# Kernel tuning notes

Hardware: AMD Instinct MI355X
Metric: run time of the kernel (lower is better)

Reference implementation:

```python
import jax, jax.numpy as jnp
import numpy as np

EMBED_DIM = 1024
NUM_HEADS = 16
HEAD_DIM = EMBED_DIM // NUM_HEADS
B, S = 4, 2048


def setup_inputs() -> dict:
    key = jax.random.key(0)
    ks = jax.random.split(key, 11)
    sc = 1.0 / np.sqrt(EMBED_DIM)
    return {
        "query": jax.random.normal(ks[0], (B, S, EMBED_DIM), jnp.float32),
        "key": jax.random.normal(ks[1], (B, S, EMBED_DIM), jnp.float32),
        "value": jax.random.normal(ks[2], (B, S, EMBED_DIM), jnp.float32),
        "Wq": jax.random.normal(ks[3], (EMBED_DIM, EMBED_DIM), jnp.float32) * sc,
        "Wk": jax.random.normal(ks[4], (EMBED_DIM, EMBED_DIM), jnp.float32) * sc,
        "Wv": jax.random.normal(ks[5], (EMBED_DIM, EMBED_DIM), jnp.float32) * sc,
        "Wo": jax.random.normal(ks[6], (EMBED_DIM, EMBED_DIM), jnp.float32) * sc,
        "bq": jax.random.normal(ks[7], (EMBED_DIM,), jnp.float32) * 0.01,
        "bk": jax.random.normal(ks[8], (EMBED_DIM,), jnp.float32) * 0.01,
        "bv": jax.random.normal(ks[9], (EMBED_DIM,), jnp.float32) * 0.01,
        "bo": jax.random.normal(ks[10], (EMBED_DIM,), jnp.float32) * 0.01,
    }


def reference(query, key, value, Wq, Wk, Wv, Wo, bq, bk, bv, bo):
    # QKV projections: [B,S,E] @ [E,E] (torch Linear uses x @ W.T; here W stored pre-transposed)
    def split_heads(x):  # [B,S,E] -> [B,H,S,D]
        Bx, Sx, _ = x.shape
        return x.reshape(Bx, Sx, NUM_HEADS, HEAD_DIM).transpose(0, 2, 1, 3)

    Q = split_heads(query @ Wq + bq)
    K = split_heads(key @ Wk + bk)
    V = split_heads(value @ Wv + bv)

    scale = 1.0 / np.sqrt(HEAD_DIM).astype(np.float32)
    scores = jnp.einsum("bhqd,bhkd->bhqk", Q, K) * scale  # [B,H,Sq,Sk]
    attn = jax.nn.softmax(scores, axis=-1)
    ctx = jnp.einsum("bhqk,bhkd->bhqd", attn, V)  # [B,H,Sq,D]
    ctx = ctx.transpose(0, 2, 1, 3).reshape(query.shape[0], query.shape[1], EMBED_DIM)
    return ctx @ Wo + bo
```

## Files before the change

### kernel.cpp

```cpp
#include <hip/hip_runtime.h>
#include <hip/hip_bf16.h>

typedef unsigned short u16;
typedef unsigned int u32;
typedef __attribute__((ext_vector_type(8))) short bf16x8;
typedef __attribute__((ext_vector_type(4))) float f32x4;
typedef __attribute__((ext_vector_type(2))) unsigned u32x2v;

constexpr int Bn = 4;
constexpr int Sn = 2048;
constexpr int En = 1024;
constexpr int Hn = 16;
constexpr int Dn = 64;
constexpr int Kd = 1024;

__device__ __forceinline__ u16 f2b(float f) {
  union { float f; unsigned u; } v; v.f = f;
  unsigned u = v.u;
  return (u16)((u + 0x7fffu + ((u >> 16) & 1u)) >> 16);
}

__device__ __forceinline__ u32 cvtpk_bf16(float lo, float hi) {
  u32 r;
  asm("v_cvt_pk_bf16_f32 %0, %1, %2" : "=v"(r) : "v"(lo), "v"(hi));
  return r;
}

__device__ __forceinline__ void gl_lds16(const u16* g, u16* l) {
  __builtin_amdgcn_global_load_lds(
      (const __attribute__((address_space(1))) void*)g,
      (__attribute__((address_space(3))) void*)l, 16, 0, 0);
}

__device__ __forceinline__ void plchain(u32& a, u32& b) {
  u32x2v s = __builtin_amdgcn_permlane32_swap(a, b, false, false);
  u32x2v t = __builtin_amdgcn_permlane16_swap(s[0], s[1], false, false);
  a = t[0]; b = t[1];
}

__device__ __forceinline__ float redmax_cross(float r) {
  union { float f; u32 u; } v; v.f = r;
  u32x2v s = __builtin_amdgcn_permlane32_swap(v.u, v.u, false, false);
  union { u32 u; float f; } x, y;
  x.u = s[0]; y.u = s[1];
  float m = fmaxf(x.f, y.f);
  union { float f; u32 u; } w; w.f = m;
  u32x2v t = __builtin_amdgcn_permlane16_swap(w.u, w.u, false, false);
  x.u = t[0]; y.u = t[1];
  return fmaxf(x.f, y.f);
}
__device__ __forceinline__ float redsum_cross(float r) {
  union { float f; u32 u; } v; v.f = r;
  u32x2v s = __builtin_amdgcn_permlane32_swap(v.u, v.u, false, false);
  union { u32 u; float f; } x, y;
  x.u = s[0]; y.u = s[1];
  float m = x.f + y.f;
  union { float f; u32 u; } w; w.f = m;
  u32x2v t = __builtin_amdgcn_permlane16_swap(w.u, w.u, false, false);
  x.u = t[0]; y.u = t[1];
  return x.f + y.f;
}

__global__ __launch_bounds__(256) void conv_act(const float* __restrict__ in,
                                                u16* __restrict__ out, int n8) {
  int i = blockIdx.x * blockDim.x + threadIdx.x;
  const int stride = gridDim.x * blockDim.x;
  for (; i < n8; i += stride) {
    const float4* p = (const float4*)(in + (size_t)i * 8);
    float4 a = p[0], b = p[1];
    union { u32 w[4]; bf16x8 v; } r;
    r.w[0] = cvtpk_bf16(a.x, a.y); r.w[1] = cvtpk_bf16(a.z, a.w);
    r.w[2] = cvtpk_bf16(b.x, b.y); r.w[3] = cvtpk_bf16(b.z, b.w);
    *(bf16x8*)(out + (size_t)i * 8) = r.v;
  }
}

__global__ __launch_bounds__(256) void conv_wt(const float* __restrict__ W,
                                               u16* __restrict__ Wt) {
  __shared__ float ts[64][65];
  const int t = threadIdx.x;
  const int k0 = blockIdx.y * 64, n0 = blockIdx.x * 64;
  const int r = t >> 4, c4 = (t & 15) * 4;
  #pragma unroll
  for (int i = 0; i < 4; i++) {
    float4 v = *(const float4*)&W[(size_t)(k0 + i * 16 + r) * En + n0 + c4];
    ts[i * 16 + r][c4 + 0] = v.x;
    ts[i * 16 + r][c4 + 1] = v.y;
    ts[i * 16 + r][c4 + 2] = v.z;
    ts[i * 16 + r][c4 + 3] = v.w;
  }
  __syncthreads();
  const int n = t >> 2, kc = (t & 3) * 16;
  u32 w8[8];
  #pragma unroll
  for (int j = 0; j < 8; j++)
    w8[j] = cvtpk_bf16(ts[kc + 2 * j][n], ts[kc + 2 * j + 1][n]);
  *(bf16x8*)&Wt[(size_t)(n0 + n) * Kd + k0 + kc]     = *(bf16x8*)&w8[0];
  *(bf16x8*)&Wt[(size_t)(n0 + n) * Kd + k0 + kc + 8] = *(bf16x8*)&w8[4];
}

template<int OUT_MODE>
__global__ __launch_bounds__(256) void gemm_k(
    const u16* __restrict__ A, const u16* __restrict__ Bt,
    const float* __restrict__ biasp, void* __restrict__ Cp, float alpha)
{
  constexpr int BK = 64;
  __shared__ u16 As[128 * BK];
  __shared__ u16 Bs[128 * BK];
  const int tid = threadIdx.x;
  const int lane = tid & 63, wave = tid >> 6;
  const int brow = blockIdx.y * 128, bcol = blockIdx.x * 128;
  const int wrow = (wave >> 1) * 64, wcol = (wave & 1) * 64;
  const int fr = lane & 15, fk = (lane >> 4) * 8, rq = (lane >> 4) * 4;

  const int lr = lane >> 3, lc = (lane & 7) * 8;
  const u16* Ag = A  + (size_t)(brow + 32 * wave + lr) * Kd + lc;
  const u16* Bg = Bt + (size_t)(bcol + 32 * wave + lr) * Kd + lc;
  u16* Asw = &As[(32 * wave) * BK];
  u16* Bsw = &Bs[(32 * wave) * BK];

  f32x4 acc[4][4] = {};

  for (int kt = 0; kt < Kd; kt += BK) {
    __syncthreads();
    #pragma unroll
    for (int i = 0; i < 4; i++) {
      gl_lds16(Ag + kt + (size_t)(8 * i) * Kd, Asw + (8 * i) * BK);
      gl_lds16(Bg + kt + (size_t)(8 * i) * Kd, Bsw + (8 * i) * BK);
    }
    __syncthreads();
    bf16x8 af[4][2], bfv[4][2];
    #pragma unroll
    for (int m = 0; m < 4; m++)
      #pragma unroll
      for (int ks = 0; ks < 2; ks++)
        af[m][ks] = *(const bf16x8*)&As[(wrow + m * 16 + fr) * BK + ks * 32 + fk];
    #pragma unroll
    for (int n = 0; n < 4; n++)
      #pragma unroll
      for (int ks = 0; ks < 2; ks++)
        bfv[n][ks] = *(const bf16x8*)&Bs[(wcol + n * 16 + fr) * BK + ks * 32 + fk];
    #pragma unroll
    for (int ks = 0; ks < 2; ks++)
      #pragma unroll
      for (int m = 0; m < 4; m++)
        #pragma unroll
        for (int n = 0; n < 4; n++)
          acc[m][n] = __builtin_amdgcn_mfma_f32_16x16x32_bf16(af[m][ks], bfv[n][ks], acc[m][n], 0, 0, 0);
  }

  #pragma unroll
  for (int m = 0; m < 4; m++) {
    #pragma unroll
    for (int n = 0; n < 4; n++) {
      const int row0 = brow + wrow + m * 16 + rq;
      const int col  = bcol + wcol + n * 16 + fr;
      const float bi = biasp[col];
      if constexpr (OUT_MODE == 0) {
        #pragma unroll
        for (int j = 0; j < 4; j++)
          ((float*)Cp)[(size_t)(row0 + j) * En + col] = (acc[m][n][j] + bi) * alpha;
      } else if constexpr (OUT_MODE == 1) {
        #pragma unroll
        for (int j = 0; j < 4; j++)
          ((u16*)Cp)[(size_t)(row0 + j) * En + col] = f2b((acc[m][n][j] + bi) * alpha);
      } else {
        u16 t4[4];
        #pragma unroll
        for (int j = 0; j < 4; j++) t4[j] = f2b((acc[m][n][j] + bi) * alpha);
        int bb = row0 >> 11, s = row0 & (Sn - 1);
        int hh = col >> 6, d = col & (Dn - 1);
        uint2 pk;
        pk.x = (u32)t4[0] | ((u32)t4[1] << 16);
        pk.y = (u32)t4[2] | ((u32)t4[3] << 16);
        *(uint2*)&((u16*)Cp)[((size_t)(bb * Hn + hh) * Dn + d) * Sn + s] = pk;
      }
    }
  }
}

#define SWZ(row, unit) (((row) * 64) + ((((unit) ^ ((row) & 7))) * 8))

__global__ __launch_bounds__(256) void attn_k(
    const u16* __restrict__ Qw, const u16* __restrict__ Kw,
    const u16* __restrict__ Vt, u16* __restrict__ Cw)
{
  constexpr int KB = 64, NT = Sn / KB, TSZ = 64 * 64;
  __shared__ u16 Ks[2 * TSZ];
  __shared__ u16 Vs[3 * TSZ];
  const int tid = threadIdx.x, lane = tid & 63, wave = tid >> 6;
  const int id = blockIdx.x;
  const int bh = (id & 7) * 8 + (id >> 7);
  const int qb = (id >> 3) & 15;
  const int b = bh >> 4, h = bh & 15;
  const int qbase = qb * 128 + wave * 32;
  const int fr = lane & 15, fk = (lane >> 4) * 8, rq = (lane >> 4) * 4;
  const int g = lane >> 4;

  const u16* Qg  = Qw + (size_t)(b * Sn + qbase) * En + h * Dn;
  const u16* Kg0 = Kw + (size_t)(b * Sn) * En + h * Dn;
  const u16* Vg0 = Vt + (size_t)bh * Dn * Sn;

  bf16x8 qf[2][2];
  #pragma unroll
  for (int qm = 0; qm < 2; qm++)
    #pragma unroll
    for (int ds = 0; ds < 2; ds++)
      qf[qm][ds] = *(const bf16x8*)&Qg[(size_t)(qm * 16 + fr) * En + ds * 32 + fk];

  float mi_s[2] = {-INFINITY, -INFINITY};
  float li_s[2] = {0.f, 0.f};
  f32x4 o[2][4] = {};

  const int sr0 = 16 * wave + (lane >> 3);
  const int su  = (lane & 7);

  auto stageK = [&](int kv, int kb) {
    #pragma unroll
    for (int c = 0; c < 2; c++) {
      const int r = sr0 + 8 * c;
      const int u = su ^ (r & 7);
      gl_lds16(Kg0 + (size_t)(kv + r) * En + u * 8, &Ks[kb * TSZ + (16 * wave + 8 * c) * 64]);
    }
  };
  auto stageV = [&](int kv, int vb) {
    #pragma unroll
    for (int c = 0; c < 2; c++) {
      const int r = sr0 + 8 * c;
      const int u = su ^ (r & 7);
      gl_lds16(Vg0 + (size_t)r * Sn + kv + u * 8, &Vs[vb * TSZ + (16 * wave + 8 * c) * 64]);
    }
  };

  stageK(0, 0); stageV(0, 0);
  asm volatile("s_waitcnt vmcnt(0)" ::: "memory");
  __syncthreads();
  stageK(KB, 1); stageV(KB, 1);

  f32x4 stc[4][2] = {};
  #pragma unroll
  for (int kb = 0; kb < 4; kb++)
    #pragma unroll
    for (int ds = 0; ds < 2; ds++) {
      bf16x8 kf = *(const bf16x8*)&Ks[SWZ(kb * 16 + fr, ds * 4 + g)];
      #pragma unroll
      for (int qm = 0; qm < 2; qm++)
        stc[kb][qm] = __builtin_amdgcn_mfma_f32_16x16x32_bf16(kf, qf[qm][ds], stc[kb][qm], 0, 0, 0);
    }

  int vcur = 0, vfut = 2;

  for (int t = 0; t < NT; t++) {
    asm volatile("s_waitcnt vmcnt(0)" ::: "memory");
    __syncthreads();

    const int kcur = t & 1;
    if (t + 2 < NT) { stageK((t + 2) * KB, kcur); stageV((t + 2) * KB, vfut); }

    f32x4 stn[4][2] = {};
    if (t + 1 < NT) {
      const u16* kbase = &Ks[(kcur ^ 1) * TSZ];
      #pragma unroll
      for (int kb = 0; kb < 4; kb++)
        #pragma unroll
        for (int ds = 0; ds < 2; ds++) {
          bf16x8 kf = *(const bf16x8*)&kbase[SWZ(kb * 16 + fr, ds * 4 + g)];
          #pragma unroll
          for (int qm = 0; qm < 2; qm++)
            stn[kb][qm] = __builtin_amdgcn_mfma_f32_16x16x32_bf16(kf, qf[qm][ds], stn[kb][qm], 0, 0, 0);
        }
    }

    bf16x8 pa[2][2];
    #pragma unroll
    for (int qm = 0; qm < 2; qm++) {
      float r = -INFINITY;
      #pragma unroll
      for (int kb = 0; kb < 4; kb++)
        #pragma unroll
        for (int j = 0; j < 4; j++) r = fmaxf(r, stc[kb][qm][j]);
      r = redmax_cross(r);
      if (!__all(r <= mi_s[qm] + 8.f)) {
        float mnew = fmaxf(mi_s[qm], r);
        float scl = __builtin_amdgcn_exp2f(mi_s[qm] - mnew);
        li_s[qm] *= scl;
        mi_s[qm] = mnew;
        #pragma unroll
        for (int j = 0; j < 4; j++) {
          float so = __shfl(scl, (lane & 0x30) | (rq + j));
          #pragma unroll
          for (int nd = 0; nd < 4; nd++) o[qm][nd][j] *= so;
        }
      }
      const float m = mi_s[qm];
      float p[4][4], sum = 0.f;
      #pragma unroll
      for (int kb = 0; kb < 4; kb++)
        #pragma unroll
        for (int j = 0; j < 4; j++) {
          p[kb][j] = __builtin_amdgcn_exp2f(stc[kb][qm][j] - m);
          sum += p[kb][j];
        }
      li_s[qm] += redsum_cross(sum);

      u32 plo[4], phi[4];
      #pragma unroll
      for (int kb = 0; kb < 4; kb++) {
        plo[kb] = cvtpk_bf16(p[kb][0], p[kb][1]);
        phi[kb] = cvtpk_bf16(p[kb][2], p[kb][3]);
      }
      plchain(plo[0], plo[1]);
      plchain(phi[0], phi[1]);
      plchain(plo[2], plo[3]);
      plchain(phi[2], phi[3]);
      union { u32 w[4]; bf16x8 v; } A0, A1;
      A0.w[0] = plo[0]; A0.w[1] = phi[0]; A0.w[2] = plo[1]; A0.w[3] = phi[1];
      A1.w[0] = plo[2]; A1.w[1] = phi[2]; A1.w[2] = plo[3]; A1.w[3] = phi[3];
      pa[qm][0] = A0.v;
      pa[qm][1] = A1.v;
    }

    {
      const u16* vbase = &Vs[vcur * TSZ];
      #pragma unroll
      for (int nd = 0; nd < 4; nd++)
        #pragma unroll
        for (int ks = 0; ks < 2; ks++) {
          bf16x8 vf = *(const bf16x8*)&vbase[SWZ(nd * 16 + fr, ks * 4 + g)];
          #pragma unroll
          for (int qm = 0; qm < 2; qm++)
            o[qm][nd] = __builtin_amdgcn_mfma_f32_16x16x32_bf16(pa[qm][ks], vf, o[qm][nd], 0, 0, 0);
        }
    }

    #pragma unroll
    for (int kb = 0; kb < 4; kb++)
      #pragma unroll
      for (int qm = 0; qm < 2; qm++)
        stc[kb][qm] = stn[kb][qm];
    vcur = (vcur == 2) ? 0 : vcur + 1;
    vfut = (vfut == 2) ? 0 : vfut + 1;
  }

  #pragma unroll
  for (int qm = 0; qm < 2; qm++) {
    float inv = 1.0f / li_s[qm];
    float rinv[4];
    #pragma unroll
    for (int j = 0; j < 4; j++) rinv[j] = __shfl(inv, (lane & 0x30) | (rq + j));
    #pragma unroll
    for (int nd = 0; nd < 4; nd++)
      #pragma unroll
      for (int j = 0; j < 4; j++) {
        int s = qbase + qm * 16 + rq + j;
        int d = nd * 16 + fr;
        Cw[((size_t)(b * Sn + s)) * En + h * Dn + d] = f2b(o[qm][nd][j] * rinv[j]);
      }
  }
}

extern "C" void kernel_launch(void* const* d_in, const int* in_sizes, int n_in,
                              void* d_out, int out_size, void* d_ws, size_t ws_size,
                              hipStream_t stream) {
  const float* q  = (const float*)d_in[0];
  const float* k  = (const float*)d_in[1];
  const float* v  = (const float*)d_in[2];
  const float* Wq = (const float*)d_in[3];
  const float* Wk = (const float*)d_in[4];
  const float* Wv = (const float*)d_in[5];
  const float* Wo = (const float*)d_in[6];
  const float* bq = (const float*)d_in[7];
  const float* bk = (const float*)d_in[8];
  const float* bv = (const float*)d_in[9];
  const float* bo = (const float*)d_in[10];

  const size_t NE = (size_t)Bn * Sn * En;
  u16* Qbf = (u16*)d_ws;
  u16* Kbf = Qbf + NE;
  u16* Vtw = Kbf + NE;
  u16* Cws = Vtw + NE;
  u16* Xact = (u16*)d_out;
  u16* WtD  = Xact + NE;
  u16* WtO  = Qbf;

  dim3 blk(256);
  dim3 gproj(En / 128, (Bn * Sn) / 128);
  dim3 gwt(16, 16);
  const int n8 = (int)(NE / 8);
  const float aq = 0.125f * 1.44269504088896340736f;

  conv_wt<<<gwt, blk, 0, stream>>>(Wq, WtD);
  conv_act<<<2048, blk, 0, stream>>>(q, Xact, n8);
  gemm_k<1><<<gproj, blk, 0, stream>>>(Xact, WtD, bq, Qbf, aq);

  conv_wt<<<gwt, blk, 0, stream>>>(Wk, WtD);
  conv_act<<<2048, blk, 0, stream>>>(k, Xact, n8);
  gemm_k<1><<<gproj, blk, 0, stream>>>(Xact, WtD, bk, Kbf, 1.0f);

  conv_wt<<<gwt, blk, 0, stream>>>(Wv, WtD);
  conv_act<<<2048, blk, 0, stream>>>(v, Xact, n8);
  gemm_k<2><<<gproj, blk, 0, stream>>>(Xact, WtD, bv, Vtw, 1.0f);

  attn_k<<<dim3(16 * Bn * Hn), blk, 0, stream>>>(Qbf, Kbf, Vtw, Cws);

  conv_wt<<<gwt, blk, 0, stream>>>(Wo, WtO);
  gemm_k<0><<<gproj, blk, 0, stream>>>(Cws, WtO, bo, d_out, 1.0f);
}
```

Baseline: 270.0 us.

## Batch weight conversions, swizzle GEMM block order, simplify attention pipelining

Converts Wq/Wk/Wv to bf16 in a single three-slice launch instead of three separate launches. Remaps GEMM blocks to a 1D grid with an XCD-aware swizzle so neighbouring tiles land on the same die for L2 reuse. Replaces the attention kernel's software-pipelined QK^T (next tile's scores computed early, with triple-buffered V) by a simpler double-buffered K/V loop that computes scores for the current tile. The simpler loop lowers register and LDS use but gives up the overlap between the score MFMAs and the softmax.

```diff
diff --git a/kernel.cpp b/kernel.cpp
--- a/kernel.cpp
+++ b/kernel.cpp
@@ -75,6 +75,34 @@
   }
 }
 
+__global__ __launch_bounds__(256) void conv_wt3(
+    const float* __restrict__ W0, const float* __restrict__ W1,
+    const float* __restrict__ W2, u16* __restrict__ T0,
+    u16* __restrict__ T1, u16* __restrict__ T2) {
+  const float* W = (blockIdx.z == 0) ? W0 : (blockIdx.z == 1) ? W1 : W2;
+  u16* Wt = (blockIdx.z == 0) ? T0 : (blockIdx.z == 1) ? T1 : T2;
+  __shared__ float ts[64][65];
+  const int t = threadIdx.x;
+  const int k0 = blockIdx.y * 64, n0 = blockIdx.x * 64;
+  const int r = t >> 4, c4 = (t & 15) * 4;
+  #pragma unroll
+  for (int i = 0; i < 4; i++) {
+    float4 v = *(const float4*)&W[(size_t)(k0 + i * 16 + r) * En + n0 + c4];
+    ts[i * 16 + r][c4 + 0] = v.x;
+    ts[i * 16 + r][c4 + 1] = v.y;
+    ts[i * 16 + r][c4 + 2] = v.z;
+    ts[i * 16 + r][c4 + 3] = v.w;
+  }
+  __syncthreads();
+  const int n = t >> 2, kc = (t & 3) * 16;
+  u32 w8[8];
+  #pragma unroll
+  for (int j = 0; j < 8; j++)
+    w8[j] = cvtpk_bf16(ts[kc + 2 * j][n], ts[kc + 2 * j + 1][n]);
+  *(bf16x8*)&Wt[(size_t)(n0 + n) * Kd + k0 + kc]     = *(bf16x8*)&w8[0];
+  *(bf16x8*)&Wt[(size_t)(n0 + n) * Kd + k0 + kc + 8] = *(bf16x8*)&w8[4];
+}
+
 __global__ __launch_bounds__(256) void conv_wt(const float* __restrict__ W,
                                                u16* __restrict__ Wt) {
   __shared__ float ts[64][65];
@@ -109,7 +137,8 @@
   __shared__ u16 Bs[128 * BK];
   const int tid = threadIdx.x;
   const int lane = tid & 63, wave = tid >> 6;
-  const int brow = blockIdx.y * 128, bcol = blockIdx.x * 128;
+  const int sid = (blockIdx.x & 7) * 64 + (blockIdx.x >> 3);
+  const int brow = (sid >> 3) * 128, bcol = (sid & 7) * 128;
   const int wrow = (wave >> 1) * 64, wcol = (wave & 1) * 64;
   const int fr = lane & 15, fk = (lane >> 4) * 8, rq = (lane >> 4) * 4;
 
@@ -187,7 +216,7 @@
 {
   constexpr int KB = 64, NT = Sn / KB, TSZ = 64 * 64;
   __shared__ u16 Ks[2 * TSZ];
-  __shared__ u16 Vs[3 * TSZ];
+  __shared__ u16 Vs[2 * TSZ];
   const int tid = threadIdx.x, lane = tid & 63, wave = tid >> 6;
   const int id = blockIdx.x;
   const int bh = (id & 7) * 8 + (id >> 7);
@@ -215,70 +244,46 @@
   const int sr0 = 16 * wave + (lane >> 3);
   const int su  = (lane & 7);
 
-  auto stageK = [&](int kv, int kb) {
+  auto stage = [&](int kv, int bufi) {
     #pragma unroll
     for (int c = 0; c < 2; c++) {
       const int r = sr0 + 8 * c;
       const int u = su ^ (r & 7);
-      gl_lds16(Kg0 + (size_t)(kv + r) * En + u * 8, &Ks[kb * TSZ + (16 * wave + 8 * c) * 64]);
+      gl_lds16(Kg0 + (size_t)(kv + r) * En + u * 8, &Ks[bufi * TSZ + (16 * wave + 8 * c) * 64]);
+      gl_lds16(Vg0 + (size_t)r * Sn + kv + u * 8,   &Vs[bufi * TSZ + (16 * wave + 8 * c) * 64]);
     }
   };
-  auto stageV = [&](int kv, int vb) {
-    #pragma unroll
-    for (int c = 0; c < 2; c++) {
-      const int r = sr0 + 8 * c;
-      const int u = su ^ (r & 7);
-      gl_lds16(Vg0 + (size_t)r * Sn + kv + u * 8, &Vs[vb * TSZ + (16 * wave + 8 * c) * 64]);
-    }
-  };
-
-  stageK(0, 0); stageV(0, 0);
-  asm volatile("s_waitcnt vmcnt(0)" ::: "memory");
-  __syncthreads();
-  stageK(KB, 1); stageV(KB, 1);
-
-  f32x4 stc[4][2] = {};
-  #pragma unroll
-  for (int kb = 0; kb < 4; kb++)
-    #pragma unroll
-    for (int ds = 0; ds < 2; ds++) {
-      bf16x8 kf = *(const bf16x8*)&Ks[SWZ(kb * 16 + fr, ds * 4 + g)];
-      #pragma unroll
-      for (int qm = 0; qm < 2; qm++)
-        stc[kb][qm] = __builtin_amdgcn_mfma_f32_16x16x32_bf16(kf, qf[qm][ds], stc[kb][qm], 0, 0, 0);
-    }
-
-  int vcur = 0, vfut = 2;
+
+  stage(0, 0);
+  int cur = 0;
 
   for (int t = 0; t < NT; t++) {
     asm volatile("s_waitcnt vmcnt(0)" ::: "memory");
     __syncthreads();
-
-    const int kcur = t & 1;
-    if (t + 2 < NT) { stageK((t + 2) * KB, kcur); stageV((t + 2) * KB, vfut); }
-
-    f32x4 stn[4][2] = {};
-    if (t + 1 < NT) {
-      const u16* kbase = &Ks[(kcur ^ 1) * TSZ];
-      #pragma unroll
-      for (int kb = 0; kb < 4; kb++)
-        #pragma unroll
-        for (int ds = 0; ds < 2; ds++) {
-          bf16x8 kf = *(const bf16x8*)&kbase[SWZ(kb * 16 + fr, ds * 4 + g)];
-          #pragma unroll
-          for (int qm = 0; qm < 2; qm++)
-            stn[kb][qm] = __builtin_amdgcn_mfma_f32_16x16x32_bf16(kf, qf[qm][ds], stn[kb][qm], 0, 0, 0);
-        }
-    }
+    if (t + 1 < NT) stage((t + 1) * KB, cur ^ 1);
+
+    f32x4 st[4][2] = {};
+    const u16* kbase = &Ks[cur * TSZ];
+    #pragma unroll
+    for (int kb = 0; kb < 4; kb++)
+      #pragma unroll
+      for (int ds = 0; ds < 2; ds++) {
+        bf16x8 kf = *(const bf16x8*)&kbase[SWZ(kb * 16 + fr, ds * 4 + g)];
+        #pragma unroll
+        for (int qm = 0; qm < 2; qm++)
+          st[kb][qm] = __builtin_amdgcn_mfma_f32_16x16x32_bf16(kf, qf[qm][ds], st[kb][qm], 0, 0, 0);
+      }
 
     bf16x8 pa[2][2];
     #pragma unroll
     for (int qm = 0; qm < 2; qm++) {
-      float r = -INFINITY;
-      #pragma unroll
-      for (int kb = 0; kb < 4; kb++)
-        #pragma unroll
-        for (int j = 0; j < 4; j++) r = fmaxf(r, stc[kb][qm][j]);
+      float r = fmaxf(fmaxf(st[0][qm][0], st[0][qm][1]),
+                      fmaxf(st[0][qm][2], st[0][qm][3]));
+      #pragma unroll
+      for (int kb = 1; kb < 4; kb++) {
+        float a1 = fmaxf(fmaxf(st[kb][qm][0], st[kb][qm][1]), st[kb][qm][2]);
+        r = fmaxf(r, fmaxf(a1, st[kb][qm][3]));
+      }
       r = redmax_cross(r);
       if (!__all(r <= mi_s[qm] + 8.f)) {
         float mnew = fmaxf(mi_s[qm], r);
@@ -298,7 +303,7 @@
       for (int kb = 0; kb < 4; kb++)
         #pragma unroll
         for (int j = 0; j < 4; j++) {
-          p[kb][j] = __builtin_amdgcn_exp2f(stc[kb][qm][j] - m);
+          p[kb][j] = __builtin_amdgcn_exp2f(st[kb][qm][j] - m);
           sum += p[kb][j];
         }
       li_s[qm] += redsum_cross(sum);
@@ -321,7 +326,7 @@
     }
 
     {
-      const u16* vbase = &Vs[vcur * TSZ];
+      const u16* vbase = &Vs[cur * TSZ];
       #pragma unroll
       for (int nd = 0; nd < 4; nd++)
         #pragma unroll
@@ -332,14 +337,7 @@
             o[qm][nd] = __builtin_amdgcn_mfma_f32_16x16x32_bf16(pa[qm][ks], vf, o[qm][nd], 0, 0, 0);
         }
     }
-
-    #pragma unroll
-    for (int kb = 0; kb < 4; kb++)
-      #pragma unroll
-      for (int qm = 0; qm < 2; qm++)
-        stc[kb][qm] = stn[kb][qm];
-    vcur = (vcur == 2) ? 0 : vcur + 1;
-    vfut = (vfut == 2) ? 0 : vfut + 1;
+    cur ^= 1;
   }
 
   #pragma unroll
@@ -375,34 +373,35 @@
   const float* bo = (const float*)d_in[10];
 
   const size_t NE = (size_t)Bn * Sn * En;
+  const size_t WE = (size_t)En * En;
   u16* Qbf = (u16*)d_ws;
   u16* Kbf = Qbf + NE;
   u16* Vtw = Kbf + NE;
   u16* Cws = Vtw + NE;
   u16* Xact = (u16*)d_out;
-  u16* WtD  = Xact + NE;
+  u16* WtQ  = Xact + NE;
+  u16* WtK  = WtQ + WE;
+  u16* WtV  = WtK + WE;
   u16* WtO  = Qbf;
 
   dim3 blk(256);
-  dim3 gproj(En / 128, (Bn * Sn) / 128);
-  dim3 gwt(16, 16);
+  dim3 gwt3(16, 16, 3);
   const int n8 = (int)(NE / 8);
   const float aq = 0.125f * 1.44269504088896340736f;
 
-  conv_wt<<<gwt, blk, 0, stream>>>(Wq, WtD);
+  conv_wt3<<<gwt3, blk, 0, stream>>>(Wq, Wk, Wv, WtQ, WtK, WtV);
+
   conv_act<<<2048, blk, 0, stream>>>(q, Xact, n8);
-  gemm_k<1><<<gproj, blk, 0, stream>>>(Xact, WtD, bq, Qbf, aq);
-
-  conv_wt<<<gwt, blk, 0, stream>>>(Wk, WtD);
+  gemm_k<1><<<512, blk, 0, stream>>>(Xact, WtQ, bq, Qbf, aq);
+
   conv_act<<<2048, blk, 0, stream>>>(k, Xact, n8);
-  gemm_k<1><<<gproj, blk, 0, stream>>>(Xact, WtD, bk, Kbf, 1.0f);
-
-  conv_wt<<<gwt, blk, 0, stream>>>(Wv, WtD);
+  gemm_k<1><<<512, blk, 0, stream>>>(Xact, WtK, bk, Kbf, 1.0f);
+
   conv_act<<<2048, blk, 0, stream>>>(v, Xact, n8);
-  gemm_k<2><<<gproj, blk, 0, stream>>>(Xact, WtD, bv, Vtw, 1.0f);
+  gemm_k<2><<<512, blk, 0, stream>>>(Xact, WtV, bv, Vtw, 1.0f);
 
   attn_k<<<dim3(16 * Bn * Hn), blk, 0, stream>>>(Qbf, Kbf, Vtw, Cws);
 
-  conv_wt<<<gwt, blk, 0, stream>>>(Wo, WtO);
-  gemm_k<0><<<gproj, blk, 0, stream>>>(Cws, WtO, bo, d_out, 1.0f);
-}
+  conv_wt<<<dim3(16, 16), blk, 0, stream>>>(Wo, WtO);
+  gemm_k<0><<<512, blk, 0, stream>>>(Cws, WtO, bo, d_out, 1.0f);
+}
```

Result: faster. 258.0 us (-4.4%).
